# Optimization experiments

Measured on AMD Instinct MI355X. Metric: run time of the kernel, lower is better.

Reference implementation:

```python
import jax, jax.numpy as jnp
import numpy as np
from jax import lax

MAX_DEG = 10
BATCH = 4096
PER_DEG = 50000              # atoms per degree bucket
N_ATOMS = PER_DEG * (MAX_DEG + 1)
F = 128                      # n_atom_features == nb_filter
EPS = 1e-5


def setup_inputs() -> dict:
    key = jax.random.key(0)
    ks = jax.random.split(key, 8)
    atoms = jax.random.normal(ks[0], (N_ATOMS, F), jnp.float32)
    # atoms sorted by degree: degree d occupies rows [d*PER_DEG, (d+1)*PER_DEG)
    deg_slice = jnp.stack([jnp.arange(MAX_DEG + 1) * PER_DEG,
                           jnp.full((MAX_DEG + 1,), PER_DEG)], axis=1).astype(jnp.int32)
    membership = jax.random.randint(ks[1], (N_ATOMS,), 0, BATCH, dtype=jnp.int32)
    inp = {"atoms": atoms, "deg_slice": deg_slice, "membership": membership}
    for d in range(1, MAX_DEG + 1):
        inp[f"adj_{d}"] = jax.random.randint(jax.random.fold_in(key, d),
                                             (PER_DEG, d), 0, N_ATOMS, dtype=jnp.int32)
    inp["W"] = jax.random.normal(ks[2], (2 * MAX_DEG + 1, F, F), jnp.float32) * 0.05
    inp["b"] = jnp.zeros((2 * MAX_DEG + 1, F), jnp.float32)
    inp["gW"] = jax.random.normal(ks[3], (MAX_DEG + 1, F, F), jnp.float32) * 0.05
    inp["gb"] = jnp.zeros((MAX_DEG + 1, F), jnp.float32)
    inp["gamma"] = jnp.ones((F,), jnp.float32)
    inp["beta"] = jnp.zeros((F,), jnp.float32)
    return inp


def reference(atoms, deg_slice, membership,
              adj_1, adj_2, adj_3, adj_4, adj_5, adj_6, adj_7, adj_8, adj_9, adj_10,
              W, b, gW, gb, gamma, beta):
    adjs = [adj_1, adj_2, adj_3, adj_4, adj_5, adj_6, adj_7, adj_8, adj_9, adj_10]
    rel_outs = [None] * (MAX_DEG + 1)
    gat_outs = [None] * (MAX_DEG + 1)
    for d in range(1, MAX_DEG + 1):
        nbr_sum = jnp.take(atoms, adjs[d - 1], axis=0).sum(axis=1)  # (PER_DEG, F)
        self_atoms = lax.dynamic_slice_in_dim(atoms, deg_slice[d, 0], PER_DEG, axis=0)
        rel_outs[d] = (nbr_sum @ W[2 * (d - 1)] + b[2 * (d - 1)]
                       + self_atoms @ W[2 * (d - 1) + 1] + b[2 * (d - 1) + 1])
        gat_outs[d] = self_atoms @ gW[d - 1] + gb[d - 1]
    # degree 0 (min_deg == 0): self transform only
    self0 = lax.dynamic_slice_in_dim(atoms, deg_slice[0, 0], PER_DEG, axis=0)
    rel_outs[0] = self0 @ W[2 * MAX_DEG] + b[2 * MAX_DEG]
    gat_outs[0] = self0 @ gW[MAX_DEG] + gb[MAX_DEG]

    activated = jnp.concatenate(rel_outs, axis=0)     # (N_ATOMS, F), degree order == atom order
    gather_atoms = jnp.concatenate(gat_outs, axis=0)  # (N_ATOMS, F)
    # graph_gather: per-molecule sum (tf.dynamic_partition + reduce_sum == segment_sum)
    graph_feat = jax.ops.segment_sum(gather_atoms, membership, num_segments=BATCH)
    # activation is 'linear' (identity); layer-norm on atom features as in call()
    m = activated.mean(axis=-1, keepdims=True)
    std = jnp.sqrt(activated.var(axis=-1, keepdims=True) + EPS)
    normed = gamma * ((activated - m) / (std + EPS)) + beta
    return normed, graph_feat
```

## Files before the change

### kernel.cpp

```cpp
#include <hip/hip_runtime.h>
#include <hip/hip_bf16.h>

#define F_DIM   128
#define PER_DEG 50000
#define NDEG    11
#define MAXD    10
#define BATCH   4096
#define N_ATOMS (PER_DEG * NDEG)

#define BM     64
#define LDSN   136
#define BPD    ((PER_DEG + BM - 1) / BM)
#define WT_K   256
#define GWT_K  1440
#define LDST_L 264
#define WT_K_L 384

typedef __attribute__((ext_vector_type(4))) float f32x4;
typedef __attribute__((ext_vector_type(8))) short short8v;
typedef __attribute__((ext_vector_type(4))) short short4v;

struct AdjPtrs { const int* p[MAXD]; };

__device__ inline short bf16bits(float x) {
    __hip_bfloat16 h = __float2bfloat16(x);
    return __builtin_bit_cast(short, h);
}
__device__ inline float bf_lo(unsigned u) { return __builtin_bit_cast(float, u << 16); }
__device__ inline float bf_hi(unsigned u) { return __builtin_bit_cast(float, u & 0xFFFF0000u); }
__device__ inline float bf2f(short s) {
    return __builtin_bit_cast(float, ((unsigned)(unsigned short)s) << 16);
}

__global__ void prep_wt_main(const float* __restrict__ W, short* __restrict__ wt) {
    int idx = blockIdx.x * blockDim.x + threadIdx.x;
    const int total = NDEG * F_DIM * WT_K;
    if (idx >= total) return;
    int d   = idx / (F_DIM * WT_K);
    int rem = idx % (F_DIM * WT_K);
    int c   = rem / WT_K;
    int k   = rem % WT_K;
    float v;
    if (d == 0) {
        v = (k < 128) ? 0.0f : W[20 * 16384 + (k - 128) * F_DIM + c];
    } else {
        int wi = (k < 128) ? (2 * (d - 1)) : (2 * (d - 1) + 1);
        v = W[wi * 16384 + (k & 127) * F_DIM + c];
    }
    wt[idx] = bf16bits(v);
}

__global__ void prep_gwt(const float* __restrict__ gW, const float* __restrict__ gb,
                         short* __restrict__ gwt) {
    int idx = blockIdx.x * blockDim.x + threadIdx.x;
    const int total = F_DIM * GWT_K;
    if (idx >= total) return;
    int c = idx / GWT_K;
    int k = idx % GWT_K;
    float v = 0.0f;
    if (k < 1408) {
        int dd = k >> 7, f = k & 127;
        int gi = dd ? (dd - 1) : 10;
        v = gW[gi * 16384 + f * F_DIM + c];
    } else if (k < 1419) {
        int dd = k - 1408;
        int gi = dd ? (dd - 1) : 10;
        v = gb[gi * F_DIM + c];
    }
    gwt[idx] = bf16bits(v);
}

__global__ void to_bf16(const float* __restrict__ in, short* __restrict__ out) {
    const size_t n8 = (size_t)N_ATOMS * F_DIM / 8;
    size_t stride = (size_t)gridDim.x * blockDim.x;
    for (size_t k = (size_t)blockIdx.x * blockDim.x + threadIdx.x; k < n8; k += stride) {
        f32x4 a = ((const f32x4*)in)[2 * k];
        f32x4 c = ((const f32x4*)in)[2 * k + 1];
        short8v o = { bf16bits(a[0]), bf16bits(a[1]), bf16bits(a[2]), bf16bits(a[3]),
                      bf16bits(c[0]), bf16bits(c[1]), bf16bits(c[2]), bf16bits(c[3]) };
        ((short8v*)out)[k] = o;
    }
}

__global__ void hist_kernel(const int* __restrict__ mem, int* __restrict__ hist2) {
    int i = blockIdx.x * blockDim.x + threadIdx.x;
    if (i >= N_ATOMS) return;
    atomicAdd(&hist2[mem[i] * NDEG + i / PER_DEG], 1);
}

__global__ void scan_offsets(const int* __restrict__ hist2,
                             int* __restrict__ off, int* __restrict__ cur) {
    __shared__ int lds[1024];
    const int tid = threadIdx.x;
    int h[4][NDEG];
    int tsum = 0;
    #pragma unroll
    for (int mi = 0; mi < 4; ++mi) {
        int m = tid * 4 + mi;
        #pragma unroll
        for (int dd = 0; dd < NDEG; ++dd) { h[mi][dd] = hist2[m * NDEG + dd]; tsum += h[mi][dd]; }
    }
    lds[tid] = tsum;
    __syncthreads();
    for (int ofs = 1; ofs < 1024; ofs <<= 1) {
        int v = (tid >= ofs) ? lds[tid - ofs] : 0;
        __syncthreads();
        lds[tid] += v;
        __syncthreads();
    }
    int run = lds[tid] - tsum;
    #pragma unroll
    for (int mi = 0; mi < 4; ++mi) {
        int m = tid * 4 + mi;
        #pragma unroll
        for (int dd = 0; dd < NDEG; ++dd) {
            int k = m * NDEG + dd;
            off[k] = run; cur[k] = run;
            run += h[mi][dd];
        }
    }
}

__global__ void scatter_kernel(const int* __restrict__ mem,
                               int* __restrict__ cur, int* __restrict__ idx) {
    int i = blockIdx.x * blockDim.x + threadIdx.x;
    if (i >= N_ATOMS) return;
    int pos = atomicAdd(&cur[mem[i] * NDEG + i / PER_DEG], 1);
    idx[pos] = i;
}

__global__ __launch_bounds__(256, 4) void fused_deg(
    const short* __restrict__ abf,
    AdjPtrs adj,
    const short* __restrict__ wt,
    const float* __restrict__ b,
    const float* __restrict__ gamma,
    const float* __restrict__ beta,
    float* __restrict__ outN)
{
    __shared__ short As[BM * LDSN];
    const int bid   = blockIdx.x;
    const int d     = bid / BPD;
    const int rb    = bid % BPD;
    const int rows0 = rb * BM;
    const int tid   = threadIdx.x;

    {
        const int rloc = tid >> 2;
        const int p    = tid & 3;
        const int grow = rows0 + rloc;
        float acc[32];
        #pragma unroll
        for (int e = 0; e < 32; ++e) acc[e] = 0.0f;
        if (grow < PER_DEG && d > 0) {
            const int* ar = adj.p[d - 1] + (size_t)grow * d;
            int idxs[MAXD];
            #pragma unroll
            for (int j = 0; j < MAXD; ++j) idxs[j] = (j < d) ? ar[j] : 0;
            #pragma unroll
            for (int j = 0; j < MAXD; ++j) {
                if (j < d) {
                    const uint4* s = (const uint4*)(abf + (size_t)idxs[j] * F_DIM) + p * 4;
                    #pragma unroll
                    for (int q = 0; q < 4; ++q) {
                        uint4 u = s[q];
                        acc[q * 8 + 0] += bf_lo(u.x); acc[q * 8 + 1] += bf_hi(u.x);
                        acc[q * 8 + 2] += bf_lo(u.y); acc[q * 8 + 3] += bf_hi(u.y);
                        acc[q * 8 + 4] += bf_lo(u.z); acc[q * 8 + 5] += bf_hi(u.z);
                        acc[q * 8 + 6] += bf_lo(u.w); acc[q * 8 + 7] += bf_hi(u.w);
                    }
                }
            }
        }
        short* basep = &As[rloc * LDSN + p * 32];
        #pragma unroll
        for (int q = 0; q < 4; ++q) {
            short8v nb = { bf16bits(acc[q * 8 + 0]), bf16bits(acc[q * 8 + 1]),
                           bf16bits(acc[q * 8 + 2]), bf16bits(acc[q * 8 + 3]),
                           bf16bits(acc[q * 8 + 4]), bf16bits(acc[q * 8 + 5]),
                           bf16bits(acc[q * 8 + 6]), bf16bits(acc[q * 8 + 7]) };
            *(short8v*)(basep + q * 8) = nb;
        }
    }
    __syncthreads();

    const int w  = tid >> 6;
    const int l  = tid & 63;
    const int cg = l & 15;
    const int rg = l >> 4;

    short8v a[8];
    const short* arow = &As[(w * 16 + cg) * LDSN + rg * 8];
    #pragma unroll
    for (int s = 0; s < 4; ++s) a[s] = *(const short8v*)(arow + s * 32);
    int srow = d * PER_DEG + rows0 + w * 16 + cg;
    if (srow >= N_ATOMS) srow = N_ATOMS - 1;
    const short* sp = abf + (size_t)srow * F_DIM + rg * 8;
    #pragma unroll
    for (int s = 0; s < 4; ++s) a[4 + s] = *(const short8v*)(sp + s * 32);

    const short* wtd = wt + (size_t)d * F_DIM * WT_K;
    f32x4 aA[8];
    #pragma unroll
    for (int n = 0; n < 8; ++n) aA[n] = 0.0f;
    #pragma unroll
    for (int s = 0; s < 8; ++s) {
        #pragma unroll
        for (int n = 0; n < 8; ++n) {
            short8v bv = *(const short8v*)(wtd + (n * 16 + cg) * WT_K + s * 32 + rg * 8);
            aA[n] = __builtin_amdgcn_mfma_f32_16x16x32_bf16(a[s], bv, aA[n], 0, 0, 0);
        }
    }

    float biasv[8], gam[8], bet[8];
    #pragma unroll
    for (int n = 0; n < 8; ++n) {
        int col = n * 16 + cg;
        biasv[n] = (d > 0) ? (b[(2 * d - 2) * F_DIM + col] + b[(2 * d - 1) * F_DIM + col])
                           : b[20 * F_DIM + col];
        gam[n] = gamma[col];
        bet[n] = beta[col];
    }
    const int valid = (PER_DEG - rows0 < BM) ? (PER_DEG - rows0) : BM;
    #pragma unroll
    for (int j = 0; j < 4; ++j) {
        const int rl = w * 16 + rg * 4 + j;
        float x[8];
        float s1 = 0.f, s2 = 0.f;
        #pragma unroll
        for (int n = 0; n < 8; ++n) {
            x[n] = aA[n][j] + biasv[n];
            s1 += x[n];
            s2 += x[n] * x[n];
        }
        #pragma unroll
        for (int m = 1; m < 16; m <<= 1) {
            s1 += __shfl_xor(s1, m);
            s2 += __shfl_xor(s2, m);
        }
        float mean = s1 * (1.0f / 128.0f);
        float var  = fmaxf(s2 * (1.0f / 128.0f) - mean * mean, 0.0f);
        float inv  = 1.0f / (sqrtf(var + 1e-5f) + 1e-5f);
        if (rl < valid) {
            float* op = outN + (size_t)(d * PER_DEG + rows0 + rl) * F_DIM;
            #pragma unroll
            for (int n = 0; n < 8; ++n)
                op[n * 16 + cg] = gam[n] * ((x[n] - mean) * inv) + bet[n];
        }
    }
}

__global__ __launch_bounds__(128) void mol_reduce(
    const short* __restrict__ abf, const int* __restrict__ idx,
    const int* __restrict__ off, const int* __restrict__ hist2,
    short* __restrict__ sums)
{
    const int m = blockIdx.x;
    const int c = threadIdx.x;
    short* out = sums + (size_t)m * GWT_K;
    for (int dd = 0; dd < NDEG; ++dd) {
        const int base = off[m * NDEG + dd];
        const int n    = hist2[m * NDEG + dd];
        float acc = 0.0f;
        #pragma unroll 4
        for (int t = 0; t < n; ++t) {
            int id = idx[base + t];
            acc += bf2f(abf[(size_t)id * F_DIM + c]);
        }
        out[dd * F_DIM + c] = bf16bits(acc);
    }
    if (c < 32)
        out[1408 + c] = (c < NDEG) ? bf16bits((float)hist2[m * NDEG + c]) : (short)0;
}

__global__ __launch_bounds__(256) void gat_gemm(
    const short* __restrict__ sums, const short* __restrict__ gwt,
    float* __restrict__ outG)
{
    const int rows0 = blockIdx.x * 64;
    const int tid = threadIdx.x;
    const int w = tid >> 6, l = tid & 63, cg = l & 15, rg = l >> 4;
    const short* ap = sums + (size_t)(rows0 + w * 16 + cg) * GWT_K + rg * 8;
    f32x4 acc[8];
    #pragma unroll
    for (int n = 0; n < 8; ++n) acc[n] = 0.0f;
    for (int ks = 0; ks < GWT_K / 32; ++ks) {
        short8v av = *(const short8v*)(ap + ks * 32);
        #pragma unroll
        for (int n = 0; n < 8; ++n) {
            short8v bv = *(const short8v*)(gwt + (size_t)(n * 16 + cg) * GWT_K + ks * 32 + rg * 8);
            acc[n] = __builtin_amdgcn_mfma_f32_16x16x32_bf16(av, bv, acc[n], 0, 0, 0);
        }
    }
    #pragma unroll
    for (int j = 0; j < 4; ++j) {
        int r = rows0 + w * 16 + rg * 4 + j;
        #pragma unroll
        for (int n = 0; n < 8; ++n)
            outG[(size_t)r * F_DIM + n * 16 + cg] = acc[n][j];
    }
}

__global__ void prep_wt_full(const float* __restrict__ W, const float* __restrict__ gW,
                             short* __restrict__ wt) {
    int idx = blockIdx.x * blockDim.x + threadIdx.x;
    const int total = NDEG * F_DIM * WT_K_L;
    if (idx >= total) return;
    int d   = idx / (F_DIM * WT_K_L);
    int rem = idx % (F_DIM * WT_K_L);
    int c   = rem / WT_K_L;
    int k   = rem % WT_K_L;
    float v;
    if (k < 256) {
        if (d == 0) v = (k < 128) ? 0.0f : W[20 * 16384 + (k - 128) * F_DIM + c];
        else {
            int wi = (k < 128) ? (2 * (d - 1)) : (2 * (d - 1) + 1);
            v = W[wi * 16384 + (k & 127) * F_DIM + c];
        }
    } else {
        int gi = (d == 0) ? 10 : (d - 1);
        v = gW[gi * 16384 + (k - 256) * F_DIM + c];
    }
    wt[idx] = bf16bits(v);
}

template<int GBF>
__global__ __launch_bounds__(256, 2) void fused_legacy(
    const float* __restrict__ atoms, const short* __restrict__ abf,
    const int* __restrict__ membership, AdjPtrs adj,
    const short* __restrict__ wt, const float* __restrict__ b,
    const float* __restrict__ gb, const float* __restrict__ gamma,
    const float* __restrict__ beta, float* __restrict__ outN, float* __restrict__ outG)
{
    __shared__ short As[BM * LDST_L];
    const int bid = blockIdx.x, d = bid / BPD, rb = bid % BPD;
    const int rows0 = rb * BM, tid = threadIdx.x;
    {
        const int rloc = tid >> 2, p = tid & 3;
        const int grow = rows0 + rloc;
        const bool rv = grow < PER_DEG;
        short* basep = &As[rloc * LDST_L + p * 32];
        if (GBF) {
            float acc[32];
            #pragma unroll
            for (int e = 0; e < 32; ++e) acc[e] = 0.0f;
            if (rv && d > 0) {
                const int* ar = adj.p[d - 1] + (size_t)grow * d;
                int idxs[MAXD];
                #pragma unroll
                for (int j = 0; j < MAXD; ++j) idxs[j] = (j < d) ? ar[j] : 0;
                #pragma unroll
                for (int j = 0; j < MAXD; ++j) if (j < d) {
                    const uint4* s = (const uint4*)(abf + (size_t)idxs[j] * F_DIM) + p * 4;
                    #pragma unroll
                    for (int q = 0; q < 4; ++q) {
                        uint4 u = s[q];
                        acc[q * 8 + 0] += bf_lo(u.x); acc[q * 8 + 1] += bf_hi(u.x);
                        acc[q * 8 + 2] += bf_lo(u.y); acc[q * 8 + 3] += bf_hi(u.y);
                        acc[q * 8 + 4] += bf_lo(u.z); acc[q * 8 + 5] += bf_hi(u.z);
                        acc[q * 8 + 6] += bf_lo(u.w); acc[q * 8 + 7] += bf_hi(u.w);
                    }
                }
            }
            #pragma unroll
            for (int q = 0; q < 4; ++q) {
                short8v nb = { bf16bits(acc[q*8+0]), bf16bits(acc[q*8+1]), bf16bits(acc[q*8+2]),
                               bf16bits(acc[q*8+3]), bf16bits(acc[q*8+4]), bf16bits(acc[q*8+5]),
                               bf16bits(acc[q*8+6]), bf16bits(acc[q*8+7]) };
                *(short8v*)(basep + q * 8) = nb;
            }
            const uint4* ss = (const uint4*)(abf + (size_t)(d * PER_DEG + grow) * F_DIM) + p * 4;
            uint4 z = {0u,0u,0u,0u};
            #pragma unroll
            for (int q = 0; q < 4; ++q) *(uint4*)(basep + 128 + q * 8) = rv ? ss[q] : z;
        } else {
            f32x4 accn[8], selfv[8];
            #pragma unroll
            for (int q = 0; q < 8; ++q) { accn[q] = 0.0f; selfv[q] = 0.0f; }
            const f32x4* atomsv = (const f32x4*)atoms;
            if (rv) {
                if (d > 0) {
                    const int* ar = adj.p[d - 1] + (size_t)grow * d;
                    int idxs[MAXD];
                    #pragma unroll
                    for (int j = 0; j < MAXD; ++j) idxs[j] = (j < d) ? ar[j] : 0;
                    #pragma unroll
                    for (int j = 0; j < MAXD; ++j) if (j < d) {
                        const f32x4* s = atomsv + (size_t)idxs[j] * 32 + p * 8;
                        #pragma unroll
                        for (int q = 0; q < 8; ++q) accn[q] += s[q];
                    }
                }
                const f32x4* s = atomsv + (size_t)(d * PER_DEG + grow) * 32 + p * 8;
                #pragma unroll
                for (int q = 0; q < 8; ++q) selfv[q] = s[q];
            }
            #pragma unroll
            for (int q = 0; q < 8; ++q) {
                short4v nb = { bf16bits(accn[q][0]), bf16bits(accn[q][1]),
                               bf16bits(accn[q][2]), bf16bits(accn[q][3]) };
                short4v sv = { bf16bits(selfv[q][0]), bf16bits(selfv[q][1]),
                               bf16bits(selfv[q][2]), bf16bits(selfv[q][3]) };
                *(short4v*)(basep + q * 4) = nb;
                *(short4v*)(basep + 128 + q * 4) = sv;
            }
        }
    }
    __syncthreads();
    const int w = tid >> 6, l = tid & 63, cg = l & 15, rg = l >> 4;
    short8v a[8];
    const short* arow = &As[(w * 16 + cg) * LDST_L + rg * 8];
    #pragma unroll
    for (int s = 0; s < 8; ++s) a[s] = *(const short8v*)(arow + s * 32);
    const short* wtd = wt + (size_t)d * F_DIM * WT_K_L;
    f32x4 aA[8], aG[8];
    #pragma unroll
    for (int n = 0; n < 8; ++n) { aA[n] = 0.0f; aG[n] = 0.0f; }
    #pragma unroll
    for (int s = 0; s < 8; ++s) {
        #pragma unroll
        for (int n = 0; n < 8; ++n) {
            short8v bv = *(const short8v*)(wtd + (n * 16 + cg) * WT_K_L + s * 32 + rg * 8);
            aA[n] = __builtin_amdgcn_mfma_f32_16x16x32_bf16(a[s], bv, aA[n], 0, 0, 0);
        }
    }
    #pragma unroll
    for (int s = 0; s < 4; ++s) {
        #pragma unroll
        for (int n = 0; n < 8; ++n) {
            short8v bv = *(const short8v*)(wtd + (n * 16 + cg) * WT_K_L + 256 + s * 32 + rg * 8);
            aG[n] = __builtin_amdgcn_mfma_f32_16x16x32_bf16(a[4 + s], bv, aG[n], 0, 0, 0);
        }
    }
    const int gi = (d == 0) ? 10 : (d - 1);
    float biasv[8], gbv[8], gam[8], bet[8];
    #pragma unroll
    for (int n = 0; n < 8; ++n) {
        int col = n * 16 + cg;
        biasv[n] = (d > 0) ? (b[(2*d-2)*F_DIM+col] + b[(2*d-1)*F_DIM+col]) : b[20*F_DIM+col];
        gbv[n] = gb[gi * F_DIM + col];
        gam[n] = gamma[col]; bet[n] = beta[col];
    }
    const int valid = (PER_DEG - rows0 < BM) ? (PER_DEG - rows0) : BM;
    #pragma unroll
    for (int j = 0; j < 4; ++j) {
        const int rl = w * 16 + rg * 4 + j;
        float x[8], s1 = 0.f, s2 = 0.f;
        #pragma unroll
        for (int n = 0; n < 8; ++n) { x[n] = aA[n][j] + biasv[n]; s1 += x[n]; s2 += x[n]*x[n]; }
        #pragma unroll
        for (int m = 1; m < 16; m <<= 1) { s1 += __shfl_xor(s1, m); s2 += __shfl_xor(s2, m); }
        float mean = s1 * (1.0f/128.0f);
        float var  = fmaxf(s2 * (1.0f/128.0f) - mean*mean, 0.0f);
        float inv  = 1.0f / (sqrtf(var + 1e-5f) + 1e-5f);
        if (rl < valid) {
            const int growi = d * PER_DEG + rows0 + rl;
            float* op = outN + (size_t)growi * F_DIM;
            float* gp = outG + (size_t)membership[growi] * F_DIM;
            #pragma unroll
            for (int n = 0; n < 8; ++n) {
                int col = n * 16 + cg;
                op[col] = gam[n] * ((x[n] - mean) * inv) + bet[n];
                atomicAdd(&gp[col], aG[n][j] + gbv[n]);
            }
        }
    }
}

extern "C" void kernel_launch(void* const* d_in, const int* in_sizes, int n_in,
                              void* d_out, int out_size, void* d_ws, size_t ws_size,
                              hipStream_t stream) {
    const float* atoms      = (const float*)d_in[0];
    const int*   membership = (const int*)d_in[2];
    AdjPtrs adj;
    for (int i = 0; i < MAXD; ++i) adj.p[i] = (const int*)d_in[3 + i];
    const float* W     = (const float*)d_in[13];
    const float* b     = (const float*)d_in[14];
    const float* gW    = (const float*)d_in[15];
    const float* gb    = (const float*)d_in[16];
    const float* gamma = (const float*)d_in[17];
    const float* beta  = (const float*)d_in[18];

    float* outN = (float*)d_out;
    float* outG = outN + (size_t)N_ATOMS * F_DIM;

    auto al = [](size_t x) { return (x + 255) & ~(size_t)255; };
    const size_t sz_wt   = al((size_t)NDEG * F_DIM * WT_K * 2);
    const size_t sz_gwt  = al((size_t)F_DIM * GWT_K * 2);
    const size_t sz_h    = al((size_t)BATCH * NDEG * 4);
    const size_t sz_idx  = al((size_t)N_ATOMS * 4);
    const size_t sz_sums = al((size_t)BATCH * GWT_K * 2);
    const size_t sz_abf  = (size_t)N_ATOMS * F_DIM * 2;

    size_t o = 0;
    short* wt    = (short*)((char*)d_ws + o); o += sz_wt;
    short* gwt   = (short*)((char*)d_ws + o); o += sz_gwt;
    int*   hist2 = (int*)  ((char*)d_ws + o); o += sz_h;
    int*   offa  = (int*)  ((char*)d_ws + o); o += sz_h;
    int*   cura  = (int*)  ((char*)d_ws + o); o += sz_h;
    int*   idx   = (int*)  ((char*)d_ws + o); o += sz_idx;
    short* sums  = (short*)((char*)d_ws + o); o += sz_sums;
    short* abf   = (short*)((char*)d_ws + o); o += sz_abf;

    if (ws_size >= o) {
        prep_wt_main<<<(NDEG * F_DIM * WT_K + 255) / 256, 256, 0, stream>>>(W, wt);
        prep_gwt<<<(F_DIM * GWT_K + 255) / 256, 256, 0, stream>>>(gW, gb, gwt);
        hipMemsetAsync(hist2, 0, (size_t)BATCH * NDEG * 4, stream);
        to_bf16<<<2048, 256, 0, stream>>>(atoms, abf);
        hist_kernel<<<(N_ATOMS + 255) / 256, 256, 0, stream>>>(membership, hist2);
        scan_offsets<<<1, 1024, 0, stream>>>(hist2, offa, cura);
        scatter_kernel<<<(N_ATOMS + 255) / 256, 256, 0, stream>>>(membership, cura, idx);
        fused_deg<<<NDEG * BPD, 256, 0, stream>>>(abf, adj, wt, b, gamma, beta, outN);
        mol_reduce<<<BATCH, 128, 0, stream>>>(abf, idx, offa, hist2, sums);
        gat_gemm<<<BATCH / 64, 256, 0, stream>>>(sums, gwt, outG);
    } else {
        short* lwt = (short*)d_ws;
        const size_t lwt_sz = al((size_t)NDEG * F_DIM * WT_K_L * 2);
        prep_wt_full<<<(NDEG * F_DIM * WT_K_L + 255) / 256, 256, 0, stream>>>(W, gW, lwt);
        hipMemsetAsync(outG, 0, (size_t)BATCH * F_DIM * 4, stream);
        if (ws_size >= lwt_sz + sz_abf) {
            short* abf2 = (short*)((char*)d_ws + lwt_sz);
            to_bf16<<<2048, 256, 0, stream>>>(atoms, abf2);
            fused_legacy<1><<<NDEG * BPD, 256, 0, stream>>>(atoms, abf2, membership, adj, lwt,
                                                            b, gb, gamma, beta, outN, outG);
        } else {
            fused_legacy<0><<<NDEG * BPD, 256, 0, stream>>>(atoms, nullptr, membership, adj, lwt,
                                                            b, gb, gamma, beta, outN, outG);
        }
    }
}
```

Baseline: 619.9 us.

## Specialize neighbor gather per degree, split mol_reduce per degree, add nontemporal hints

The neighbor gather is templated on degree so each block runs a fully unrolled loop with no per-iteration predicate, and the adjacency indices are read with nontemporal loads. Launch bounds on fused_deg are raised to 6 blocks per CU to allow more waves in flight for the latency-bound gather. mol_reduce now launches one block per (molecule, degree) pair instead of one per molecule looping over 11 degrees, which adds parallelism for the serial per-molecule reduction. The fp32 input load in to_bf16 and the normalized output store also use nontemporal hints to avoid polluting the cache. The higher occupancy target may force register spilling in the GEMM part of fused_deg.

```diff
diff --git a/kernel.cpp b/kernel.cpp
--- a/kernel.cpp
+++ b/kernel.cpp
@@ -74,8 +74,8 @@
     const size_t n8 = (size_t)N_ATOMS * F_DIM / 8;
     size_t stride = (size_t)gridDim.x * blockDim.x;
     for (size_t k = (size_t)blockIdx.x * blockDim.x + threadIdx.x; k < n8; k += stride) {
-        f32x4 a = ((const f32x4*)in)[2 * k];
-        f32x4 c = ((const f32x4*)in)[2 * k + 1];
+        f32x4 a = __builtin_nontemporal_load((const f32x4*)in + 2 * k);
+        f32x4 c = __builtin_nontemporal_load((const f32x4*)in + 2 * k + 1);
         short8v o = { bf16bits(a[0]), bf16bits(a[1]), bf16bits(a[2]), bf16bits(a[3]),
                       bf16bits(c[0]), bf16bits(c[1]), bf16bits(c[2]), bf16bits(c[3]) };
         ((short8v*)out)[k] = o;
@@ -129,7 +129,29 @@
     idx[pos] = i;
 }
 
-__global__ __launch_bounds__(256, 4) void fused_deg(
+template<int D>
+__device__ __forceinline__ void gather_nbrs(const short* __restrict__ abf,
+                                            const int* __restrict__ ar, int p,
+                                            float* __restrict__ acc) {
+    int idxs[D];
+    #pragma unroll
+    for (int j = 0; j < D; ++j)
+        idxs[j] = __builtin_nontemporal_load(ar + j);
+    #pragma unroll
+    for (int j = 0; j < D; ++j) {
+        const uint4* rp = (const uint4*)(abf + (size_t)idxs[j] * F_DIM) + p * 4;
+        #pragma unroll
+        for (int q = 0; q < 4; ++q) {
+            uint4 u = rp[q];
+            acc[q * 8 + 0] += bf_lo(u.x); acc[q * 8 + 1] += bf_hi(u.x);
+            acc[q * 8 + 2] += bf_lo(u.y); acc[q * 8 + 3] += bf_hi(u.y);
+            acc[q * 8 + 4] += bf_lo(u.z); acc[q * 8 + 5] += bf_hi(u.z);
+            acc[q * 8 + 6] += bf_lo(u.w); acc[q * 8 + 7] += bf_hi(u.w);
+        }
+    }
+}
+
+__global__ __launch_bounds__(256, 6) void fused_deg(
     const short* __restrict__ abf,
     AdjPtrs adj,
     const short* __restrict__ wt,
@@ -154,22 +176,17 @@
         for (int e = 0; e < 32; ++e) acc[e] = 0.0f;
         if (grow < PER_DEG && d > 0) {
             const int* ar = adj.p[d - 1] + (size_t)grow * d;
-            int idxs[MAXD];
-            #pragma unroll
-            for (int j = 0; j < MAXD; ++j) idxs[j] = (j < d) ? ar[j] : 0;
-            #pragma unroll
-            for (int j = 0; j < MAXD; ++j) {
-                if (j < d) {
-                    const uint4* s = (const uint4*)(abf + (size_t)idxs[j] * F_DIM) + p * 4;
-                    #pragma unroll
-                    for (int q = 0; q < 4; ++q) {
-                        uint4 u = s[q];
-                        acc[q * 8 + 0] += bf_lo(u.x); acc[q * 8 + 1] += bf_hi(u.x);
-                        acc[q * 8 + 2] += bf_lo(u.y); acc[q * 8 + 3] += bf_hi(u.y);
-                        acc[q * 8 + 4] += bf_lo(u.z); acc[q * 8 + 5] += bf_hi(u.z);
-                        acc[q * 8 + 6] += bf_lo(u.w); acc[q * 8 + 7] += bf_hi(u.w);
-                    }
-                }
+            switch (d) {
+                case 1:  gather_nbrs<1>(abf, ar, p, acc); break;
+                case 2:  gather_nbrs<2>(abf, ar, p, acc); break;
+                case 3:  gather_nbrs<3>(abf, ar, p, acc); break;
+                case 4:  gather_nbrs<4>(abf, ar, p, acc); break;
+                case 5:  gather_nbrs<5>(abf, ar, p, acc); break;
+                case 6:  gather_nbrs<6>(abf, ar, p, acc); break;
+                case 7:  gather_nbrs<7>(abf, ar, p, acc); break;
+                case 8:  gather_nbrs<8>(abf, ar, p, acc); break;
+                case 9:  gather_nbrs<9>(abf, ar, p, acc); break;
+                default: gather_nbrs<10>(abf, ar, p, acc); break;
             }
         }
         short* basep = &As[rloc * LDSN + p * 32];
@@ -245,7 +262,8 @@
             float* op = outN + (size_t)(d * PER_DEG + rows0 + rl) * F_DIM;
             #pragma unroll
             for (int n = 0; n < 8; ++n)
-                op[n * 16 + cg] = gam[n] * ((x[n] - mean) * inv) + bet[n];
+                __builtin_nontemporal_store(gam[n] * ((x[n] - mean) * inv) + bet[n],
+                                            op + n * 16 + cg);
         }
     }
 }
@@ -255,22 +273,22 @@
     const int* __restrict__ off, const int* __restrict__ hist2,
     short* __restrict__ sums)
 {
-    const int m = blockIdx.x;
-    const int c = threadIdx.x;
+    const int key = blockIdx.x;
+    const int m   = key / NDEG;
+    const int dd  = key - m * NDEG;
+    const int c   = threadIdx.x;
+    const int base = off[key];
+    const int n    = hist2[key];
+    float acc = 0.0f;
+    #pragma unroll 4
+    for (int t = 0; t < n; ++t) {
+        int id = idx[base + t];
+        acc += bf2f(abf[(size_t)id * F_DIM + c]);
+    }
     short* out = sums + (size_t)m * GWT_K;
-    for (int dd = 0; dd < NDEG; ++dd) {
-        const int base = off[m * NDEG + dd];
-        const int n    = hist2[m * NDEG + dd];
-        float acc = 0.0f;
-        #pragma unroll 4
-        for (int t = 0; t < n; ++t) {
-            int id = idx[base + t];
-            acc += bf2f(abf[(size_t)id * F_DIM + c]);
-        }
-        out[dd * F_DIM + c] = bf16bits(acc);
-    }
-    if (c < 32)
-        out[1408 + c] = (c < NDEG) ? bf16bits((float)hist2[m * NDEG + c]) : (short)0;
+    out[dd * F_DIM + c] = bf16bits(acc);
+    if (c == 0) out[1408 + dd] = bf16bits((float)n);
+    if (dd == 0 && c >= 11 && c < 32) out[1408 + c] = 0;
 }
 
 __global__ __launch_bounds__(256) void gat_gemm(
@@ -511,7 +529,7 @@
         scan_offsets<<<1, 1024, 0, stream>>>(hist2, offa, cura);
         scatter_kernel<<<(N_ATOMS + 255) / 256, 256, 0, stream>>>(membership, cura, idx);
         fused_deg<<<NDEG * BPD, 256, 0, stream>>>(abf, adj, wt, b, gamma, beta, outN);
-        mol_reduce<<<BATCH, 128, 0, stream>>>(abf, idx, offa, hist2, sums);
+        mol_reduce<<<BATCH * NDEG, 128, 0, stream>>>(abf, idx, offa, hist2, sums);
         gat_gemm<<<BATCH / 64, 256, 0, stream>>>(sums, gwt, outG);
     } else {
         short* lwt = (short*)d_ws;
```

Measured after the change: 988.9 us. 59.5% more time.
